# Kernel optimization log

Measured on AMD Instinct MI355X. Metric: run time of the kernel, lower is better.

## Reference

```python
import jax, jax.numpy as jnp
import numpy as np

N, NB, D, F, E, NUM_RBF = 50000, 256, 128, 16, 800000, 15
EPS = 1e-7
NEG = 0.01
MAX_LEN = 5.0


def _glorot(k, shape):
    return jax.random.normal(k, shape, dtype=jnp.float32) / np.float32(np.sqrt(shape[0]))


def setup_inputs() -> dict:
    key = jax.random.key(0)
    ks = jax.random.split(key, 32)
    inp = {}
    inp['h_A'] = jax.random.normal(ks[0], (N, D), jnp.float32)
    inp['v_A'] = jax.random.normal(ks[1], (N, F, 3), jnp.float32)
    inp['x_A'] = jax.random.normal(ks[2], (N, 3), jnp.float32) * 3.0
    inp['h_B'] = jax.random.normal(ks[3], (NB, D), jnp.float32)
    inp['mask'] = jnp.ones((N, NB), jnp.float32)
    inp['src'] = jax.random.randint(ks[4], (E,), 0, N, dtype=jnp.int32)
    inp['dst'] = jax.random.randint(ks[5], (E,), 0, N, dtype=jnp.int32)
    inp['rbf_k'] = jnp.array([0.5], jnp.float32)
    inp['W_rbf1'] = _glorot(ks[6], (NUM_RBF, D)); inp['b_rbf1'] = jnp.zeros((D,), jnp.float32)
    inp['W_rbf2'] = _glorot(ks[7], (NUM_RBF, F)); inp['b_rbf2'] = jnp.zeros((F,), jnp.float32)
    inp['W_rbf3'] = _glorot(ks[8], (NUM_RBF, F)); inp['b_rbf3'] = jnp.zeros((F,), jnp.float32)
    inp['vn1_W'] = _glorot(ks[9], (F, F)); inp['vn1_U'] = _glorot(ks[10], (F, F))
    inp['vn2_W'] = _glorot(ks[11], (F, F)); inp['vn2_U'] = _glorot(ks[12], (F, F))
    inp['vn3_W'] = _glorot(ks[13], (F, F)); inp['vn3_U'] = _glorot(ks[14], (F, F))
    inp['phi1_W'] = _glorot(ks[15], (D + F, D)); inp['phi1_b'] = jnp.zeros((D,), jnp.float32)
    inp['phi2_W'] = _glorot(ks[16], (D + F, F)); inp['phi2_b'] = jnp.zeros((F,), jnp.float32)
    inp['phi3_W'] = _glorot(ks[17], (D, F)); inp['phi3_b'] = jnp.zeros((F,), jnp.float32)
    inp['Wq'] = _glorot(ks[18], (D, D)); inp['Wk'] = _glorot(ks[19], (D, D))
    inp['Wv'] = _glorot(ks[20], (D, D)); inp['bv'] = jnp.zeros((D,), jnp.float32)
    inp['gru_Wih'] = _glorot(ks[21], (3 * D, 2 * D)) * 0.5
    inp['gru_Whh'] = _glorot(ks[22], (3 * D, D)) * 0.5
    inp['gru_bih'] = jnp.zeros((3 * D,), jnp.float32)
    inp['gru_bhh'] = jnp.zeros((3 * D,), jnp.float32)
    inp['vmlp_W1'] = _glorot(ks[23], (2 * F, 2 * F)); inp['vmlp_U1'] = _glorot(ks[24], (2 * F, 2 * F))
    inp['vmlp_W2'] = _glorot(ks[25], (F, 2 * F))
    return inp


def _forward(h_A, v_A, x_A, h_B, mask, src, dst, rbf_k, W_rbf1, b_rbf1, W_rbf2, b_rbf2,
             W_rbf3, b_rbf3, vn1_W, vn1_U, vn2_W, vn2_U, vn3_W, vn3_U, phi1_W, phi1_b,
             phi2_W, phi2_b, phi3_W, phi3_b, Wq, Wk, Wv, bv, gru_Wih, gru_Whh, gru_bih,
             gru_bhh, vmlp_W1, vmlp_U1, vmlp_W2):
    lrelu = lambda x: jax.nn.leaky_relu(x, NEG)

    def vn_relu(v, W, U):  # Vector Neuron linear + VN-ReLU; v: [n, f, 3]
        q = jnp.einsum('gf,nfc->ngc', W, v)
        k = jnp.einsum('gf,nfc->ngc', U, v)
        dot = jnp.sum(q * k, -1, keepdims=True)
        ksq = jnp.sum(k * k, -1, keepdims=True) + EPS
        return jnp.where(dot >= 0, q, q - (dot / ksq) * k)

    # --- per-node mixed scalar/vector features (generate_mixed_features) ---
    vnorm1 = jnp.linalg.norm(vn_relu(v_A, vn1_W, vn1_U), axis=2) + EPS  # [N,F]
    vnorm2 = jnp.linalg.norm(vn_relu(v_A, vn2_W, vn2_U), axis=2) + EPS
    hp = lrelu(jnp.concatenate([h_A, vnorm1], 1) @ phi1_W + phi1_b)     # [N,D]
    hpp = lrelu(jnp.concatenate([h_A, vnorm2], 1) @ phi2_W + phi2_b)    # [N,F]
    vp = vn_relu(v_A, vn3_W, vn3_U) * lrelu(h_A @ phi3_W + phi3_b)[:, :, None]  # [N,F,3]

    # --- cross attention A <- B ---
    q = lrelu(h_A @ Wq)
    kk = lrelu(h_B @ Wk)
    vv = h_B @ Wv + bv
    a = mask * (q @ kk.T) - 1000.0 * (1.0 - mask)                       # [N,NB]
    attn = jax.nn.softmax(a, axis=1) @ vv                               # [N,D]

    # --- edge-wise RBF expansion + point convolution messages ---
    r_ij = x_A[src] - x_A[dst]                                          # [E,3]
    rnorm = jnp.linalg.norm(r_ij, axis=1, keepdims=True)                # [E,1]
    centers = jnp.linspace(0.0, MAX_LEN, NUM_RBF, dtype=jnp.float32)
    rbf = jnp.exp(-jnp.square(rnorm - centers) * rbf_k)                 # [E,R]
    rbf_h = rbf @ W_rbf1 + b_rbf1                                       # [E,D]
    rbf_v1 = rbf @ W_rbf2 + b_rbf2                                      # [E,F]
    rbf_v2 = rbf @ W_rbf3 + b_rbf3                                      # [E,F]
    msg_h = rbf_h * hp[dst]                                             # [E,D]
    # einsum('ef,ef,ec->efc', rbf_v2, hpp_dst, r_ij)
    msg_v = rbf_v1[:, :, None] * vp[dst] + (rbf_v2 * hpp[dst])[:, :, None] * r_ij[:, None, :]

    # --- mean aggregation at destination nodes (update_all copy_e + mean) ---
    n_nodes = h_A.shape[0]
    cnt = jax.ops.segment_sum(jnp.ones((src.shape[0],), msg_h.dtype), dst, num_segments=n_nodes)
    den = jnp.maximum(cnt, 1.0)
    agg_h = jax.ops.segment_sum(msg_h, dst, num_segments=n_nodes) / den[:, None]
    agg_v = jax.ops.segment_sum(msg_v, dst, num_segments=n_nodes) / den[:, None, None]

    # --- GRUCell(2D, D): input = [h, cross_attn], hidden = aggregated message ---
    x_in = jnp.concatenate([h_A, attn], -1)                             # [N,2D]
    gi = x_in @ gru_Wih.T + gru_bih
    gh = agg_h @ gru_Whh.T + gru_bhh
    Dh = h_A.shape[1]
    r = jax.nn.sigmoid(gi[:, :Dh] + gh[:, :Dh])
    z = jax.nn.sigmoid(gi[:, Dh:2 * Dh] + gh[:, Dh:2 * Dh])
    n = jnp.tanh(gi[:, 2 * Dh:] + r * gh[:, 2 * Dh:])
    node_upd = h_A + ((1.0 - z) * n + z * agg_h)

    # --- vector update via Vector_MLP(2F -> F) with residual ---
    vin = jnp.concatenate([v_A, agg_v], axis=1)                         # [N,2F,3]
    vh = vn_relu(vin, vmlp_W1, vmlp_U1)
    v_evolved = v_A + jnp.einsum('gf,nfc->ngc', vmlp_W2, vh)            # [N,F,3]
    return v_evolved, node_upd


def reference(h_A, v_A, x_A, h_B, mask, src, dst, rbf_k, W_rbf1, b_rbf1, W_rbf2, b_rbf2,
              W_rbf3, b_rbf3, vn1_W, vn1_U, vn2_W, vn2_U, vn3_W, vn3_U, phi1_W, phi1_b,
              phi2_W, phi2_b, phi3_W, phi3_b, Wq, Wk, Wv, bv, gru_Wih, gru_Whh, gru_bih,
              gru_bhh, vmlp_W1, vmlp_U1, vmlp_W2):
    return _forward(h_A, v_A, x_A, h_B, mask, src, dst, rbf_k, W_rbf1, b_rbf1, W_rbf2,
                    b_rbf2, W_rbf3, b_rbf3, vn1_W, vn1_U, vn2_W, vn2_U, vn3_W, vn3_U,
                    phi1_W, phi1_b, phi2_W, phi2_b, phi3_W, phi3_b, Wq, Wk, Wv, bv,
                    gru_Wih, gru_Whh, gru_bih, gru_bhh, vmlp_W1, vmlp_U1, vmlp_W2)
```

## Files before the change

### kernel.cpp

```cpp
#include <hip/hip_runtime.h>
#include <math.h>

#define NN 50000
#define NBB 256
#define DD 128
#define FF 16
#define EE 800000
#define RR 15
#define EPSV 1e-7f
#define CSPACE (5.0f/14.0f)
#define NBLK 782

__device__ __forceinline__ float lrelu(float x){ return x >= 0.f ? x : 0.01f*x; }
__device__ __forceinline__ float sigmoidf_(float x){ return 1.f/(1.f+expf(-x)); }

typedef __bf16 bf16x8 __attribute__((ext_vector_type(8)));
typedef float f32x4 __attribute__((ext_vector_type(4)));

__device__ __forceinline__ unsigned short f2bf(float x){
    union { float f; unsigned int u; } a; a.f = x;
    unsigned int r = (a.u + 0x7fffu + ((a.u >> 16) & 1u)) >> 16;
    return (unsigned short)r;
}
__device__ __forceinline__ unsigned int pack2(float a, float b){
    return (unsigned int)f2bf(a) | ((unsigned int)f2bf(b) << 16);
}
// ... 261 lines not shown
                float* vo = vpO + (size_t)n*48 + lr*3;
                vo[0] = o[0]*gate; vo[1] = o[1]*gate; vo[2] = o[2]*gate;
            }
        }
    } else {
        float b2 = phi2b[lr];
        #pragma unroll
        for (int r4 = 0; r4 < 4; ++r4){
            int nl = (wv-4)*16 + lg*4 + r4;
            int n = n0 + nl;
            if (n < NN) hppO[(size_t)n*FF + lr] = lrelu(a23[r4] + b2);
        }
    }
}

__global__ __launch_bounds__(512, 4) void k_attn_mfma(
    const unsigned short* __restrict__ hAB, const unsigned short* __restrict__ pWq,
    const unsigned short* __restrict__ pKK, const unsigned short* __restrict__ pVV,
    const float* __restrict__ mask, unsigned short* __restrict__ attnB)
{
    __shared__ unsigned short sU[64*256];
    __shared__ float sMx[64][2];
    __shared__ float sSm[64][2];
    unsigned short* sX = sU;
    unsigned short* sQ = sU + 64*128;
    unsigned short* sP = sU;
    unsigned short* sImg = sU;
    int tid = threadIdx.x;
    int n0 = blockIdx.x*64;

    #pragma unroll
    for (int it = 0; it < 2; ++it){
        int i = tid + it*512;
        ((uint4*)sX)[i] = ((const uint4*)hAB)[(size_t)blockIdx.x*1024 + i];
    }
    __syncthreads();

    int wv = tid>>6, l = tid&63, lr = l&15, lg = l>>4;
    int rw = wv>>1, chh = wv&1;
    int rowA = rw*16 + lr;

    {
        f32x4 q[4];
        #pragma unroll
        for (int c = 0; c < 4; ++c) q[c] = (f32x4){0.f,0.f,0.f,0.f};
        for (int kt = 0; kt < 4; ++kt){
            bf16x8 a = ld8(&sX[rowA*128 + (((kt*4+lg) ^ (rowA&7))*8)]);
            #pragma unroll
            for (int c = 0; c < 4; ++c){
                bf16x8 b = ld8(pWq + (size_t)(((chh*4+c)*4 + kt)*512) + l*8);
                q[c] = __builtin_amdgcn_mfma_f32_16x16x32_bf16(a, b, q[c], 0, 0, 0);
            }
        }
        __syncthreads();
        #pragma unroll
        for (int c = 0; c < 4; ++c)
        #pragma unroll
        for (int r4 = 0; r4 < 4; ++r4){
            int row = rw*16 + lg*4 + r4;
            int col = chh*64 + c*16 + lr;
            int cb = col>>3;
            sQ[row*128 + ((cb ^ (row&7))*8) + (col&7)] = f2bf(lrelu(q[c][r4]));
        }
    }
    __syncthreads();

    f32x4 S[8];
    #pragma unroll
    for (int cl = 0; cl < 8; ++cl) S[cl] = (f32x4){0.f,0.f,0.f,0.f};
    for (int kt = 0; kt < 4; ++kt){
        bf16x8 a = ld8(&sQ[rowA*128 + (((kt*4+lg) ^ (rowA&7))*8)]);
        #pragma unroll
        for (int cl = 0; cl < 8; ++cl){
            bf16x8 b = ld8(pKK + (size_t)(((chh*8+cl)*4 + kt)*512) + l*8);
            S[cl] = __builtin_amdgcn_mfma_f32_16x16x32_bf16(a, b, S[cl], 0, 0, 0);
        }
    }
    float den[4];
    #pragma unroll
    for (int r4 = 0; r4 < 4; ++r4){
        int row = rw*16 + lg*4 + r4;
        int gn = n0 + row; if (gn > NN-1) gn = NN-1;
        float mx = -1e30f;
        #pragma unroll
        for (int cl = 0; cl < 8; ++cl){
            int col = chh*128 + cl*16 + lr;
            float m = mask[(size_t)gn*NBB + col];
            float s = m*S[cl][r4] - 1000.f*(1.f-m);
            S[cl][r4] = s;
            mx = fmaxf(mx, s);
        }
        mx = fmaxf(mx, __shfl_xor(mx, 1));
        mx = fmaxf(mx, __shfl_xor(mx, 2));
        mx = fmaxf(mx, __shfl_xor(mx, 4));
        mx = fmaxf(mx, __shfl_xor(mx, 8));
        if (lr == 0) sMx[row][chh] = mx;
    }
    __syncthreads();
    #pragma unroll
    for (int r4 = 0; r4 < 4; ++r4){
        int row = rw*16 + lg*4 + r4;
        float m = fmaxf(sMx[row][0], sMx[row][1]);
        float sm = 0.f;
        #pragma unroll
        for (int cl = 0; cl < 8; ++cl){
            float p = expf(S[cl][r4] - m);
            S[cl][r4] = p;
            sm += p;
        }
        sm += __shfl_xor(sm, 1);
        sm += __shfl_xor(sm, 2);
        sm += __shfl_xor(sm, 4);
        sm += __shfl_xor(sm, 8);
        if (lr == 0) sSm[row][chh] = sm;
    }
    __syncthreads();
    #pragma unroll
    for (int r4 = 0; r4 < 4; ++r4){
        int row = rw*16 + lg*4 + r4;
        den[r4] = sSm[row][0] + sSm[row][1];
    }
    #pragma unroll
    for (int cl = 0; cl < 8; ++cl)
    #pragma unroll
    for (int r4 = 0; r4 < 4; ++r4){
        int row = rw*16 + lg*4 + r4;
        int col = chh*128 + cl*16 + lr;
        int cb = col>>3;
        sP[row*256 + ((cb ^ (row&7))*8) + (col&7)] = f2bf(S[cl][r4]);
    }
    __syncthreads();

    f32x4 O[4];
    #pragma unroll
    for (int c = 0; c < 4; ++c) O[c] = (f32x4){0.f,0.f,0.f,0.f};
    for (int kt = 0; kt < 8; ++kt){
        bf16x8 a = ld8(&sP[rowA*256 + (((kt*4+lg) ^ (rowA&7))*8)]);
        #pragma unroll
        for (int c = 0; c < 4; ++c){
            bf16x8 b = ld8(pVV + (size_t)(((chh*4+c)*8 + kt)*512) + l*8);
            O[c] = __builtin_amdgcn_mfma_f32_16x16x32_bf16(a, b, O[c], 0, 0, 0);
        }
    }
    __syncthreads();
    #pragma unroll
    for (int c = 0; c < 4; ++c)
    #pragma unroll
    for (int r4 = 0; r4 < 4; ++r4){
        int row = rw*16 + lg*4 + r4;
        int col = chh*64 + c*16 + lr;
        sImg[row*128 + (((col>>3) ^ (row&7))*8) + (col&7)] = f2bf(O[c][r4] / den[r4]);
    }
    __syncthreads();
    #pragma unroll
    for (int it = 0; it < 2; ++it){
        int i = tid + it*512;
        ((uint4*)attnB)[(size_t)blockIdx.x*1024 + i] = ((const uint4*)sImg)[i];
    }
}

__global__ __launch_bounds__(256) void k_hist(const int* __restrict__ dst, int* __restrict__ deg){
    int e = blockIdx.x*256 + threadIdx.x;
    if (e < EE) atomicAdd(&deg[dst[e]], 1);
}

__global__ __launch_bounds__(256) void k_scan1(const int* __restrict__ deg,
                                               int* __restrict__ excl, int* __restrict__ bsum){
    __shared__ int s[256];
    int tid = threadIdx.x;
    int i = blockIdx.x*256 + tid;
    int v = (i < NN) ? deg[i] : 0;
    s[tid] = v;
    __syncthreads();
    for (int o = 1; o < 256; o <<= 1){
        int t = 0;
// ... 28 lines not shown
        start[i] = st;
        cursor[i] = st;
    }
    if (i == 0) start[NN] = EE;
}

__global__ __launch_bounds__(256) void k_scatter(const int* __restrict__ src,
                                                 const int* __restrict__ dst,
                                                 int* __restrict__ cursor, int* __restrict__ esrc){
    int e = blockIdx.x*256 + threadIdx.x;
    if (e >= EE) return;
    int pos = atomicAdd(&cursor[dst[e]], 1);
    esrc[pos] = src[e];
}

__global__ __launch_bounds__(256) void k_gather(const int* __restrict__ start,
                                                const int* __restrict__ esrc,
                                                const float* __restrict__ xA,
                                                const float* __restrict__ rbf_k,
                                                float* __restrict__ acc)
{
    int gt = blockIdx.x*256 + threadIdx.x;
    int n = gt >> 2, sub = gt & 3;
    if (n >= NN) return;
    float kc = rbf_k[0];
    float xd0 = xA[n*3+0], xd1 = xA[n*3+1], xd2 = xA[n*3+2];
    float a[64];
    #pragma unroll
    for (int i = 0; i < 64; ++i) a[i] = 0.f;
    int b0 = start[n], b1 = start[n+1];
    for (int i = b0 + sub; i < b1; i += 4){
        int s = esrc[i];
        float r0 = xA[s*3+0]-xd0, r1 = xA[s*3+1]-xd1, r2 = xA[s*3+2]-xd2;
        float rn = sqrtf(r0*r0+r1*r1+r2*r2);
        a[0] += 1.f;
        a[16] += r0; a[17] += r1; a[18] += r2;
        #pragma unroll
        for (int q = 0; q < RR; ++q){
            float df = rn - (float)q*CSPACE;
            float rb = expf(-df*df*kc);
            a[1+q] += rb;
            a[19+q*3+0] += rb*r0;
            a[19+q*3+1] += rb*r1;
            a[19+q*3+2] += rb*r2;
        }
    }
    #pragma unroll
    for (int i = 0; i < 64; ++i){
        a[i] += __shfl_xor(a[i], 1);
        a[i] += __shfl_xor(a[i], 2);
    }
    float4* o = (float4*)(acc + (size_t)n*64);
    #pragma unroll
    for (int i = 0; i < 4; ++i){
        int idx = sub*4 + i;
        o[idx] = make_float4(a[4*idx], a[4*idx+1], a[4*idx+2], a[4*idx+3]);
    }
}

__global__ __launch_bounds__(512) void k_gru_mfma(
    const unsigned short* __restrict__ hAB, const unsigned short* __restrict__ attnB,
    const unsigned short* __restrict__ hpB, const float* __restrict__ acc,
    const unsigned short* __restrict__ pWr1,
    const unsigned short* __restrict__ pWih, const unsigned short* __restrict__ pWhh,
    const float* __restrict__ bih, const float* __restrict__ bhh,
    float* __restrict__ outNode)
{
    __shared__ unsigned short sX[64*256];
    __shared__ unsigned short sGm[64*128];
    __shared__ float sCnt[64];
    unsigned short* sM = sGm;
    int tid = threadIdx.x;
    int n0 = blockIdx.x*64;

    #pragma unroll
    for (int it = 0; it < 2; ++it){
        int i = tid + it*512;
        uint4 v = ((const uint4*)hAB)[(size_t)blockIdx.x*1024 + i];
        int row = i >> 4, p = i & 15;
        *(uint4*)&sX[row*256 + p*8] = v;
    }
    #pragma unroll
    for (int it = 0; it < 2; ++it){
        int i = tid + it*512;
        uint4 v = ((const uint4*)attnB)[(size_t)blockIdx.x*1024 + i];
        int row = i >> 4, p = i & 15;
        *(uint4*)&sX[row*256 + 128 + p*8] = v;
    }
    #pragma unroll
    for (int it = 0; it < 4; ++it){
        int i = tid + it*512;
        int row = i >> 5, k = i & 31;
        int gn = n0 + row; if (gn > NN-1) gn = NN-1;
        float v = (k < 16) ? acc[(size_t)gn*64 + k] : 0.f;
        sM[row*40 + k] = f2bf(v);
        if (k == 0) sCnt[row] = v;
    }
    __syncthreads();

    int wv = tid >> 6, l = tid & 63;
    int lr = l & 15, lg = l >> 4;
    int col = wv*16 + lr;

    {
        f32x4 sv[4];
        #pragma unroll
        for (int rt = 0; rt < 4; ++rt) sv[rt] = (f32x4){0.f,0.f,0.f,0.f};
        bf16x8 b = ld8(pWr1 + (size_t)wv*512 + l*8);
        #pragma unroll
        for (int rt = 0; rt < 4; ++rt){
            int row = rt*16 + lr;
            bf16x8 a = ld8(&sM[row*40 + lg*8]);
            sv[rt] = __builtin_amdgcn_mfma_f32_16x16x32_bf16(a, b, sv[rt], 0, 0, 0);
        }
        __syncthreads();
        #pragma unroll
        for (int rt = 0; rt < 4; ++rt){
            #pragma unroll
            for (int r4 = 0; r4 < 4; ++r4){
                int row = rt*16 + lg*4 + r4;
                int gn = n0 + row; if (gn > NN-1) gn = NN-1;
                float cnt = sCnt[row];
                float den = fmaxf(cnt, 1.f);
                float g = bf2f(hpB[(size_t)gn*DD + col]) * sv[rt][r4] / den;
                sGm[row*128 + (((col>>3) ^ (row&7))*8) + (col&7)] = f2bf(g);
            }
        }
    }
    __syncthreads();

    f32x4 aR[4], aZ[4], aNI[4], aNH[4];
    #pragma unroll
    for (int rt = 0; rt < 4; ++rt){
        aR[rt] = (f32x4){0.f,0.f,0.f,0.f};
        aZ[rt] = (f32x4){0.f,0.f,0.f,0.f};
        aNI[rt] = (f32x4){0.f,0.f,0.f,0.f};
        aNH[rt] = (f32x4){0.f,0.f,0.f,0.f};
    }
    const unsigned short* bR = pWih + ((size_t)(0*8 + wv)*8)*512 + l*8;
    const unsigned short* bZ = pWih + ((size_t)(1*8 + wv)*8)*512 + l*8;
    const unsigned short* bN = pWih + ((size_t)(2*8 + wv)*8)*512 + l*8;
    for (int kt = 0; kt < 8; ++kt){
        bf16x8 br_ = ld8(bR + kt*512);
        bf16x8 bz_ = ld8(bZ + kt*512);
        bf16x8 bn_ = ld8(bN + kt*512);
        #pragma unroll
        for (int rt = 0; rt < 4; ++rt){
            int rowA = rt*16 + lr;
            bf16x8 a = ld8(&sX[rowA*256 + (((kt*4 + lg) ^ (rowA&7))*8)]);
            aR[rt]  = __builtin_amdgcn_mfma_f32_16x16x32_bf16(a, br_, aR[rt], 0, 0, 0);
            aZ[rt]  = __builtin_amdgcn_mfma_f32_16x16x32_bf16(a, bz_, aZ[rt], 0, 0, 0);
            aNI[rt] = __builtin_amdgcn_mfma_f32_16x16x32_bf16(a, bn_, aNI[rt], 0, 0, 0);
        }
    }
    const unsigned short* cR = pWhh + ((size_t)(0*8 + wv)*4)*512 + l*8;
    const unsigned short* cZ = pWhh + ((size_t)(1*8 + wv)*4)*512 + l*8;
    const unsigned short* cN = pWhh + ((size_t)(2*8 + wv)*4)*512 + l*8;
    for (int kt = 0; kt < 4; ++kt){
        bf16x8 br_ = ld8(cR + kt*512);
        bf16x8 bz_ = ld8(cZ + kt*512);
        bf16x8 bn_ = ld8(cN + kt*512);
        #pragma unroll
        for (int rt = 0; rt < 4; ++rt){
            int rowA = rt*16 + lr;
            bf16x8 a = ld8(&sGm[rowA*128 + (((kt*4 + lg) ^ (rowA&7))*8)]);
            aR[rt]  = __builtin_amdgcn_mfma_f32_16x16x32_bf16(a, br_, aR[rt], 0, 0, 0);
            aZ[rt]  = __builtin_amdgcn_mfma_f32_16x16x32_bf16(a, bz_, aZ[rt], 0, 0, 0);
            aNH[rt] = __builtin_amdgcn_mfma_f32_16x16x32_bf16(a, bn_, aNH[rt], 0, 0, 0);
        }
    }

    float b_r = bih[col] + bhh[col];
    float b_z = bih[DD+col] + bhh[DD+col];
    float b_ni = bih[2*DD+col];
    float b_nh = bhh[2*DD+col];
    #pragma unroll
    for (int rt = 0; rt < 4; ++rt){
        #pragma unroll
        for (int r4 = 0; r4 < 4; ++r4){
            int nl = rt*16 + lg*4 + r4;
            int n = n0 + nl;
            if (n < NN){
                float rg = sigmoidf_(aR[rt][r4] + b_r);
                float zg = sigmoidf_(aZ[rt][r4] + b_z);
                float ng = tanhf(aNI[rt][r4] + b_ni + rg*(aNH[rt][r4] + b_nh));
                float sg = bf2f(sGm[nl*128 + (((col>>3) ^ (nl&7))*8) + (col&7)]);
                float h = bf2f(sX[nl*256 + (((col>>3) ^ (nl&7))*8) + (col&7)]);
                outNode[(size_t)n*DD + col] = h + (1.f-zg)*ng + zg*sg;
            }
        }
    }
}

__global__ __launch_bounds__(256) void k_vec(
    const float* __restrict__ vA, const float* __restrict__ vp,
    const float* __restrict__ hpp, const float* __restrict__ acc,
    const float* __restrict__ Wr2, const float* __restrict__ br2,
    const float* __restrict__ Wr3, const float* __restrict__ br3,
    const float* __restrict__ W1, const float* __restrict__ U1,
    const float* __restrict__ W2, float* __restrict__ outV)
{
    __shared__ float sW1[32*32], sU1[32*32], sW2[16*32];
    __shared__ float sWr2[RR*FF], sWr3[RR*FF];
    __shared__ float sVin[8][32][3];
    __shared__ float sVh[8][32][3];
    __shared__ float sAcc[8][64];
    __shared__ float sVA[8][48];
    int tid = threadIdx.x;
    for (int i = tid; i < 1024; i += 256){ sW1[i]=W1[i]; sU1[i]=U1[i]; }
    for (int i = tid; i < 512; i += 256) sW2[i]=W2[i];
    for (int i = tid; i < RR*FF; i += 256){ sWr2[i]=Wr2[i]; sWr3[i]=Wr3[i]; }
    int n0 = blockIdx.x*8;
    for (int i = tid; i < 8*64; i += 256) sAcc[i/64][i%64] = acc[(size_t)n0*64 + i];
    for (int i = tid; i < 8*48; i += 256) sVA[i/48][i%48] = vA[(size_t)n0*48 + i];
    __syncthreads();
    int t = tid >> 5, g = tid & 31;
    int n = n0 + t;
    if (g < 16){
        int f = g;
        float cnt = sAcc[t][0];
        float den = fmaxf(cnt, 1.f);
        float s1 = cnt*br2[f];
        #pragma unroll
        for (int r = 0; r < RR; ++r) s1 += sAcc[t][1+r]*sWr2[r*FF+f];
        float hpv = hpp[(size_t)n*FF+f];
        float b3 = br3[f];
        #pragma unroll
        for (int c = 0; c < 3; ++c){
            float s2 = b3*sAcc[t][16+c];
            #pragma unroll
            for (int r = 0; r < RR; ++r) s2 += sAcc[t][19+r*3+c]*sWr3[r*FF+f];
            float aggv = (vp[(size_t)n*48 + f*3 + c]*s1 + hpv*s2)/den;
            sVin[t][FF+f][c] = aggv;
            sVin[t][f][c] = sVA[t][f*3+c];
        }
    }
    __syncthreads();
    {
        float q0=0,q1=0,q2=0,k0=0,k1=0,k2=0;
        #pragma unroll
        for (int ff = 0; ff < 32; ++ff){
            int f = (ff + g) & 31;
            float w = sW1[g*32+f], u = sU1[g*32+f];
            float v0=sVin[t][f][0], v1=sVin[t][f][1], v2=sVin[t][f][2];
            q0+=w*v0;q1+=w*v1;q2+=w*v2;
            k0+=u*v0;k1+=u*v1;k2+=u*v2;
        }
        float dot=q0*k0+q1*k1+q2*k2;
        float ksq=k0*k0+k1*k1+k2*k2+EPSV;
        float s = dot>=0.f?0.f:dot/ksq;
        sVh[t][g][0]=q0-s*k0; sVh[t][g][1]=q1-s*k1; sVh[t][g][2]=q2-s*k2;
    }
    __syncthreads();
    if (g < 16){
        float o0=sVA[t][g*3+0], o1=sVA[t][g*3+1], o2=sVA[t][g*3+2];
        #pragma unroll
        for (int ff = 0; ff < 32; ++ff){
            int f = (ff + g) & 31;
            float w = sW2[g*32+f];
            o0 += w*sVh[t][f][0];
            o1 += w*sVh[t][f][1];
            o2 += w*sVh[t][f][2];
        }
        outV[(size_t)n*48 + g*3 + 0] = o0;
        outV[(size_t)n*48 + g*3 + 1] = o1;
        outV[(size_t)n*48 + g*3 + 2] = o2;
    }
}

extern "C" void kernel_launch(void* const* d_in, const int* in_sizes, int n_in,
                              void* d_out, int out_size, void* d_ws, size_t ws_size,
                              hipStream_t stream)
{
    const float* hA   = (const float*)d_in[0];
    const float* vA   = (const float*)d_in[1];
    const float* xA   = (const float*)d_in[2];
    const float* hB   = (const float*)d_in[3];
// ... 55 lines not shown
    int* esrc   = (int*)ws;  ws += EE;

    float* outV = (float*)d_out;
    float* outH = (float*)d_out + (size_t)NN*FF*3;

    const int NB_SCAN = (NN + 255)/256;

    k_prep<<<512, 256, 0, stream>>>(Wih, Whh, Wq, phi1W, phi2W, phi3W, Wr1, br1,
                                    hB, Wk, Wv, bv,
                                    pWih, pWhh, pWq, pPhi1, pPhi2, pPhi3, pWr1,
                                    pKK, pVV, deg);
    k_hist<<<(EE+255)/256, 256, 0, stream>>>(dst, deg);
    k_scan1<<<NB_SCAN, 256, 0, stream>>>(deg, excl, bsum);
    k_scan23<<<NB_SCAN, 256, 0, stream>>>(excl, bsum, NB_SCAN, startN, cursor);
    k_scatter<<<(EE+255)/256, 256, 0, stream>>>(src, dst, cursor, esrc);
    k_gather<<<(NN*4+255)/256, 256, 0, stream>>>(startN, esrc, xA, rbfk, acc);
    k_node<<<NBLK, 512, 0, stream>>>(hA, vA, vn1W, vn1U, vn2W, vn2U, vn3W, vn3U,
                                     pPhi1, phi1b, pPhi2, phi2b, pPhi3, phi3b,
                                     hpB, hpp, vp, hAB);
    k_attn_mfma<<<NBLK, 512, 0, stream>>>(hAB, pWq, pKK, pVV, mask, attnB);
    k_gru_mfma<<<NBLK, 512, 0, stream>>>(hAB, attnB, hpB, acc, pWr1,
                                         pWih, pWhh, bih, bhh, outH);
    k_vec<<<NN/8, 256, 0, stream>>>(vA, vp, hpp, acc, Wr2, br2, Wr3, br3, W1, U1, W2, outV);
}
```

Before: 336.8 us.

## Merge independent kernels into shared launches via block-range dispatch

Combines the edge gather with the attention kernel, and the GRU with the vector-update kernel, into single launches. Block index ranges pick which workload each block runs. The goal is to cut launch count and let independent work fill the GPU at the same time, removing tail idle time between kernels. In exchange, each fused kernel uses the larger of the two register and shared-memory footprints, and the attention part loses its launch_bounds occupancy hint, which may lower occupancy.

Result: slower. 344.0 us (+2.1%).

```diff
diff --git a/kernel.cpp b/kernel.cpp
--- a/kernel.cpp
+++ b/kernel.cpp
@@ -10,6 +10,8 @@
 #define EPSV 1e-7f
 #define CSPACE (5.0f/14.0f)
 #define NBLK 782
+#define NGA 391
+#define NVB 3125
 
 __device__ __forceinline__ float lrelu(float x){ return x >= 0.f ? x : 0.01f*x; }
 __device__ __forceinline__ float sigmoidf_(float x){ return 1.f/(1.f+expf(-x)); }
@@ -301,151 +303,6 @@
     }
 }
 
-__global__ __launch_bounds__(512, 4) void k_attn_mfma(
-    const unsigned short* __restrict__ hAB, const unsigned short* __restrict__ pWq,
-    const unsigned short* __restrict__ pKK, const unsigned short* __restrict__ pVV,
-    const float* __restrict__ mask, unsigned short* __restrict__ attnB)
-{
-    __shared__ unsigned short sU[64*256];
-    __shared__ float sMx[64][2];
-    __shared__ float sSm[64][2];
-    unsigned short* sX = sU;
-    unsigned short* sQ = sU + 64*128;
-    unsigned short* sP = sU;
-    unsigned short* sImg = sU;
-    int tid = threadIdx.x;
-    int n0 = blockIdx.x*64;
-
-    #pragma unroll
-    for (int it = 0; it < 2; ++it){
-        int i = tid + it*512;
-        ((uint4*)sX)[i] = ((const uint4*)hAB)[(size_t)blockIdx.x*1024 + i];
-    }
-    __syncthreads();
-
-    int wv = tid>>6, l = tid&63, lr = l&15, lg = l>>4;
-    int rw = wv>>1, chh = wv&1;
-    int rowA = rw*16 + lr;
-
-    {
-        f32x4 q[4];
-        #pragma unroll
-        for (int c = 0; c < 4; ++c) q[c] = (f32x4){0.f,0.f,0.f,0.f};
-        for (int kt = 0; kt < 4; ++kt){
-            bf16x8 a = ld8(&sX[rowA*128 + (((kt*4+lg) ^ (rowA&7))*8)]);
-            #pragma unroll
-            for (int c = 0; c < 4; ++c){
-                bf16x8 b = ld8(pWq + (size_t)(((chh*4+c)*4 + kt)*512) + l*8);
-                q[c] = __builtin_amdgcn_mfma_f32_16x16x32_bf16(a, b, q[c], 0, 0, 0);
-            }
-        }
-        __syncthreads();
-        #pragma unroll
-        for (int c = 0; c < 4; ++c)
-        #pragma unroll
-        for (int r4 = 0; r4 < 4; ++r4){
-            int row = rw*16 + lg*4 + r4;
-            int col = chh*64 + c*16 + lr;
-            int cb = col>>3;
-            sQ[row*128 + ((cb ^ (row&7))*8) + (col&7)] = f2bf(lrelu(q[c][r4]));
-        }
-    }
-    __syncthreads();
-
-    f32x4 S[8];
-    #pragma unroll
-    for (int cl = 0; cl < 8; ++cl) S[cl] = (f32x4){0.f,0.f,0.f,0.f};
-    for (int kt = 0; kt < 4; ++kt){
-        bf16x8 a = ld8(&sQ[rowA*128 + (((kt*4+lg) ^ (rowA&7))*8)]);
-        #pragma unroll
-        for (int cl = 0; cl < 8; ++cl){
-            bf16x8 b = ld8(pKK + (size_t)(((chh*8+cl)*4 + kt)*512) + l*8);
-            S[cl] = __builtin_amdgcn_mfma_f32_16x16x32_bf16(a, b, S[cl], 0, 0, 0);
-        }
-    }
-    float den[4];
-    #pragma unroll
-    for (int r4 = 0; r4 < 4; ++r4){
-        int row = rw*16 + lg*4 + r4;
-        int gn = n0 + row; if (gn > NN-1) gn = NN-1;
-        float mx = -1e30f;
-        #pragma unroll
-        for (int cl = 0; cl < 8; ++cl){
-            int col = chh*128 + cl*16 + lr;
-            float m = mask[(size_t)gn*NBB + col];
-            float s = m*S[cl][r4] - 1000.f*(1.f-m);
-            S[cl][r4] = s;
-            mx = fmaxf(mx, s);
-        }
-        mx = fmaxf(mx, __shfl_xor(mx, 1));
-        mx = fmaxf(mx, __shfl_xor(mx, 2));
-        mx = fmaxf(mx, __shfl_xor(mx, 4));
-        mx = fmaxf(mx, __shfl_xor(mx, 8));
-        if (lr == 0) sMx[row][chh] = mx;
-    }
-    __syncthreads();
-    #pragma unroll
-    for (int r4 = 0; r4 < 4; ++r4){
-        int row = rw*16 + lg*4 + r4;
-        float m = fmaxf(sMx[row][0], sMx[row][1]);
-        float sm = 0.f;
-        #pragma unroll
-        for (int cl = 0; cl < 8; ++cl){
-            float p = expf(S[cl][r4] - m);
-            S[cl][r4] = p;
-            sm += p;
-        }
-        sm += __shfl_xor(sm, 1);
-        sm += __shfl_xor(sm, 2);
-        sm += __shfl_xor(sm, 4);
-        sm += __shfl_xor(sm, 8);
-        if (lr == 0) sSm[row][chh] = sm;
-    }
-    __syncthreads();
-    #pragma unroll
-    for (int r4 = 0; r4 < 4; ++r4){
-        int row = rw*16 + lg*4 + r4;
-        den[r4] = sSm[row][0] + sSm[row][1];
-    }
-    #pragma unroll
-    for (int cl = 0; cl < 8; ++cl)
-    #pragma unroll
-    for (int r4 = 0; r4 < 4; ++r4){
-        int row = rw*16 + lg*4 + r4;
-        int col = chh*128 + cl*16 + lr;
-        int cb = col>>3;
-        sP[row*256 + ((cb ^ (row&7))*8) + (col&7)] = f2bf(S[cl][r4]);
-    }
-    __syncthreads();
-
-    f32x4 O[4];
-    #pragma unroll
-    for (int c = 0; c < 4; ++c) O[c] = (f32x4){0.f,0.f,0.f,0.f};
-    for (int kt = 0; kt < 8; ++kt){
-        bf16x8 a = ld8(&sP[rowA*256 + (((kt*4+lg) ^ (rowA&7))*8)]);
-        #pragma unroll
-        for (int c = 0; c < 4; ++c){
-            bf16x8 b = ld8(pVV + (size_t)(((chh*4+c)*8 + kt)*512) + l*8);
-            O[c] = __builtin_amdgcn_mfma_f32_16x16x32_bf16(a, b, O[c], 0, 0, 0);
-        }
-    }
-    __syncthreads();
-    #pragma unroll
-    for (int c = 0; c < 4; ++c)
-    #pragma unroll
-    for (int r4 = 0; r4 < 4; ++r4){
-        int row = rw*16 + lg*4 + r4;
-        int col = chh*64 + c*16 + lr;
-        sImg[row*128 + (((col>>3) ^ (row&7))*8) + (col&7)] = f2bf(O[c][r4] / den[r4]);
-    }
-    __syncthreads();
-    #pragma unroll
-    for (int it = 0; it < 2; ++it){
-        int i = tid + it*512;
-        ((uint4*)attnB)[(size_t)blockIdx.x*1024 + i] = ((const uint4*)sImg)[i];
-    }
-}
-
 __global__ __launch_bounds__(256) void k_hist(const int* __restrict__ dst, int* __restrict__ deg){
     int e = blockIdx.x*256 + threadIdx.x;
     if (e < EE) atomicAdd(&deg[dst[e]], 1);
@@ -504,225 +361,374 @@
     esrc[pos] = src[e];
 }
 
-__global__ __launch_bounds__(256) void k_gather(const int* __restrict__ start,
-                                                const int* __restrict__ esrc,
-                                                const float* __restrict__ xA,
-                                                const float* __restrict__ rbf_k,
-                                                float* __restrict__ acc)
+__global__ __launch_bounds__(512) void k_ga_attn(
+    const int* __restrict__ start, const int* __restrict__ esrc,
+    const float* __restrict__ xA, const float* __restrict__ rbf_k,
+    float* __restrict__ acc,
+    const unsigned short* __restrict__ hAB, const unsigned short* __restrict__ pWq,
+    const unsigned short* __restrict__ pKK, const unsigned short* __restrict__ pVV,
+    const float* __restrict__ mask, unsigned short* __restrict__ attnB)
 {
-    int gt = blockIdx.x*256 + threadIdx.x;
-    int n = gt >> 2, sub = gt & 3;
-    if (n >= NN) return;
-    float kc = rbf_k[0];
-    float xd0 = xA[n*3+0], xd1 = xA[n*3+1], xd2 = xA[n*3+2];
-    float a[64];
-    #pragma unroll
-    for (int i = 0; i < 64; ++i) a[i] = 0.f;
-    int b0 = start[n], b1 = start[n+1];
-    for (int i = b0 + sub; i < b1; i += 4){
-        int s = esrc[i];
-        float r0 = xA[s*3+0]-xd0, r1 = xA[s*3+1]-xd1, r2 = xA[s*3+2]-xd2;
-        float rn = sqrtf(r0*r0+r1*r1+r2*r2);
-        a[0] += 1.f;
-        a[16] += r0; a[17] += r1; a[18] += r2;
-        #pragma unroll
-        for (int q = 0; q < RR; ++q){
-            float df = rn - (float)q*CSPACE;
-            float rb = expf(-df*df*kc);
-            a[1+q] += rb;
-            a[19+q*3+0] += rb*r0;
-            a[19+q*3+1] += rb*r1;
-            a[19+q*3+2] += rb*r2;
-        }
-    }
-    #pragma unroll
-    for (int i = 0; i < 64; ++i){
-        a[i] += __shfl_xor(a[i], 1);
-        a[i] += __shfl_xor(a[i], 2);
-    }
-    float4* o = (float4*)(acc + (size_t)n*64);
-    #pragma unroll
-    for (int i = 0; i < 4; ++i){
-        int idx = sub*4 + i;
-        o[idx] = make_float4(a[4*idx], a[4*idx+1], a[4*idx+2], a[4*idx+3]);
-    }
-}
-
-__global__ __launch_bounds__(512) void k_gru_mfma(
+    __shared__ __align__(16) unsigned char smem[33792];
+    int tid = threadIdx.x;
+    if (blockIdx.x < NGA){
+        int gt = blockIdx.x*512 + tid;
+        int n = gt >> 2, sub = gt & 3;
+        if (n >= NN) return;
+        float kc = rbf_k[0];
+        float xd0 = xA[n*3+0], xd1 = xA[n*3+1], xd2 = xA[n*3+2];
+        float a[64];
+        #pragma unroll
+        for (int i = 0; i < 64; ++i) a[i] = 0.f;
+        int b0 = start[n], b1 = start[n+1];
+        for (int i = b0 + sub; i < b1; i += 4){
+            int s = esrc[i];
+            float r0 = xA[s*3+0]-xd0, r1 = xA[s*3+1]-xd1, r2 = xA[s*3+2]-xd2;
+            float rn = sqrtf(r0*r0+r1*r1+r2*r2);
+            a[0] += 1.f;
+            a[16] += r0; a[17] += r1; a[18] += r2;
+            #pragma unroll
+            for (int q = 0; q < RR; ++q){
+                float df = rn - (float)q*CSPACE;
+                float rb = expf(-df*df*kc);
+                a[1+q] += rb;
+                a[19+q*3+0] += rb*r0;
+                a[19+q*3+1] += rb*r1;
+                a[19+q*3+2] += rb*r2;
+            }
+        }
+        #pragma unroll
+        for (int i = 0; i < 64; ++i){
+            a[i] += __shfl_xor(a[i], 1);
+            a[i] += __shfl_xor(a[i], 2);
+        }
+        float4* o = (float4*)(acc + (size_t)n*64);
+        #pragma unroll
+        for (int i = 0; i < 4; ++i){
+            int idx = sub*4 + i;
+            o[idx] = make_float4(a[4*idx], a[4*idx+1], a[4*idx+2], a[4*idx+3]);
+        }
+        return;
+    }
+    int ab = blockIdx.x - NGA;
+    unsigned short* sU = (unsigned short*)smem;
+    float* sMx = (float*)(smem + 32768);
+    float* sSm = (float*)(smem + 33280);
+    unsigned short* sX = sU;
+    unsigned short* sQ = sU + 64*128;
+    unsigned short* sP = sU;
+    unsigned short* sImg = sU;
+    int n0 = ab*64;
+
+    #pragma unroll
+    for (int it = 0; it < 2; ++it){
+        int i = tid + it*512;
+        ((uint4*)sX)[i] = ((const uint4*)hAB)[(size_t)ab*1024 + i];
+    }
+    __syncthreads();
+
+    int wv = tid>>6, l = tid&63, lr = l&15, lg = l>>4;
+    int rw = wv>>1, chh = wv&1;
+    int rowA = rw*16 + lr;
+
+    {
+        f32x4 q[4];
+        #pragma unroll
+        for (int c = 0; c < 4; ++c) q[c] = (f32x4){0.f,0.f,0.f,0.f};
+        for (int kt = 0; kt < 4; ++kt){
+            bf16x8 a = ld8(&sX[rowA*128 + (((kt*4+lg) ^ (rowA&7))*8)]);
+            #pragma unroll
+            for (int c = 0; c < 4; ++c){
+                bf16x8 b = ld8(pWq + (size_t)(((chh*4+c)*4 + kt)*512) + l*8);
+                q[c] = __builtin_amdgcn_mfma_f32_16x16x32_bf16(a, b, q[c], 0, 0, 0);
+            }
+        }
+        __syncthreads();
+        #pragma unroll
+        for (int c = 0; c < 4; ++c)
+        #pragma unroll
+        for (int r4 = 0; r4 < 4; ++r4){
+            int row = rw*16 + lg*4 + r4;
+            int col = chh*64 + c*16 + lr;
+            int cb = col>>3;
+            sQ[row*128 + ((cb ^ (row&7))*8) + (col&7)] = f2bf(lrelu(q[c][r4]));
+        }
+    }
+    __syncthreads();
+
+    f32x4 S[8];
+    #pragma unroll
+    for (int cl = 0; cl < 8; ++cl) S[cl] = (f32x4){0.f,0.f,0.f,0.f};
+    for (int kt = 0; kt < 4; ++kt){
+        bf16x8 a = ld8(&sQ[rowA*128 + (((kt*4+lg) ^ (rowA&7))*8)]);
+        #pragma unroll
+        for (int cl = 0; cl < 8; ++cl){
+            bf16x8 b = ld8(pKK + (size_t)(((chh*8+cl)*4 + kt)*512) + l*8);
+            S[cl] = __builtin_amdgcn_mfma_f32_16x16x32_bf16(a, b, S[cl], 0, 0, 0);
+        }
+    }
+    float den[4];
+    #pragma unroll
+    for (int r4 = 0; r4 < 4; ++r4){
+        int row = rw*16 + lg*4 + r4;
+        int gn = n0 + row; if (gn > NN-1) gn = NN-1;
+        float mx = -1e30f;
+        #pragma unroll
+        for (int cl = 0; cl < 8; ++cl){
+            int col = chh*128 + cl*16 + lr;
+            float m = mask[(size_t)gn*NBB + col];
+            float s = m*S[cl][r4] - 1000.f*(1.f-m);
+            S[cl][r4] = s;
+            mx = fmaxf(mx, s);
+        }
+        mx = fmaxf(mx, __shfl_xor(mx, 1));
+        mx = fmaxf(mx, __shfl_xor(mx, 2));
+        mx = fmaxf(mx, __shfl_xor(mx, 4));
+        mx = fmaxf(mx, __shfl_xor(mx, 8));
+        if (lr == 0) sMx[row*2+chh] = mx;
+    }
+    __syncthreads();
+    #pragma unroll
+    for (int r4 = 0; r4 < 4; ++r4){
+        int row = rw*16 + lg*4 + r4;
+        float m = fmaxf(sMx[row*2+0], sMx[row*2+1]);
+        float sm = 0.f;
+        #pragma unroll
+        for (int cl = 0; cl < 8; ++cl){
+            float p = expf(S[cl][r4] - m);
+            S[cl][r4] = p;
+            sm += p;
+        }
+        sm += __shfl_xor(sm, 1);
+        sm += __shfl_xor(sm, 2);
+        sm += __shfl_xor(sm, 4);
+        sm += __shfl_xor(sm, 8);
+        if (lr == 0) sSm[row*2+chh] = sm;
+    }
+    __syncthreads();
+    #pragma unroll
+    for (int r4 = 0; r4 < 4; ++r4){
+        int row = rw*16 + lg*4 + r4;
+        den[r4] = sSm[row*2+0] + sSm[row*2+1];
+    }
+    #pragma unroll
+    for (int cl = 0; cl < 8; ++cl)
+    #pragma unroll
+    for (int r4 = 0; r4 < 4; ++r4){
+        int row = rw*16 + lg*4 + r4;
+        int col = chh*128 + cl*16 + lr;
+        int cb = col>>3;
+        sP[row*256 + ((cb ^ (row&7))*8) + (col&7)] = f2bf(S[cl][r4]);
+    }
+    __syncthreads();
+
+    f32x4 O[4];
+    #pragma unroll
+    for (int c = 0; c < 4; ++c) O[c] = (f32x4){0.f,0.f,0.f,0.f};
+    for (int kt = 0; kt < 8; ++kt){
+        bf16x8 a = ld8(&sP[rowA*256 + (((kt*4+lg) ^ (rowA&7))*8)]);
+        #pragma unroll
+        for (int c = 0; c < 4; ++c){
+            bf16x8 b = ld8(pVV + (size_t)(((chh*4+c)*8 + kt)*512) + l*8);
+            O[c] = __builtin_amdgcn_mfma_f32_16x16x32_bf16(a, b, O[c], 0, 0, 0);
+        }
+    }
+    __syncthreads();
+    #pragma unroll
+    for (int c = 0; c < 4; ++c)
+    #pragma unroll
+    for (int r4 = 0; r4 < 4; ++r4){
+        int row = rw*16 + lg*4 + r4;
+        int col = chh*64 + c*16 + lr;
+        sImg[row*128 + (((col>>3) ^ (row&7))*8) + (col&7)] = f2bf(O[c][r4] / den[r4]);
+    }
+    __syncthreads();
+    #pragma unroll
+    for (int it = 0; it < 2; ++it){
+        int i = tid + it*512;
+        ((uint4*)attnB)[(size_t)ab*1024 + i] = ((const uint4*)sImg)[i];
+    }
+}
+
+__global__ __launch_bounds__(512) void k_gru_vec(
     const unsigned short* __restrict__ hAB, const unsigned short* __restrict__ attnB,
     const unsigned short* __restrict__ hpB, const float* __restrict__ acc,
     const unsigned short* __restrict__ pWr1,
     const unsigned short* __restrict__ pWih, const unsigned short* __restrict__ pWhh,
     const float* __restrict__ bih, const float* __restrict__ bhh,
-    float* __restrict__ outNode)
-{
-    __shared__ unsigned short sX[64*256];
-    __shared__ unsigned short sGm[64*128];
-    __shared__ float sCnt[64];
-    unsigned short* sM = sGm;
-    int tid = threadIdx.x;
-    int n0 = blockIdx.x*64;
-
-    #pragma unroll
-    for (int it = 0; it < 2; ++it){
-        int i = tid + it*512;
-        uint4 v = ((const uint4*)hAB)[(size_t)blockIdx.x*1024 + i];
-        int row = i >> 4, p = i & 15;
-        *(uint4*)&sX[row*256 + p*8] = v;
-    }
-    #pragma unroll
-    for (int it = 0; it < 2; ++it){
-        int i = tid + it*512;
-        uint4 v = ((const uint4*)attnB)[(size_t)blockIdx.x*1024 + i];
-        int row = i >> 4, p = i & 15;
-        *(uint4*)&sX[row*256 + 128 + p*8] = v;
-    }
-    #pragma unroll
-    for (int it = 0; it < 4; ++it){
-        int i = tid + it*512;
-        int row = i >> 5, k = i & 31;
-        int gn = n0 + row; if (gn > NN-1) gn = NN-1;
-        float v = (k < 16) ? acc[(size_t)gn*64 + k] : 0.f;
-        sM[row*40 + k] = f2bf(v);
-        if (k == 0) sCnt[row] = v;
-    }
-    __syncthreads();
-
-    int wv = tid >> 6, l = tid & 63;
-    int lr = l & 15, lg = l >> 4;
-    int col = wv*16 + lr;
-
-    {
-        f32x4 sv[4];
-        #pragma unroll
-        for (int rt = 0; rt < 4; ++rt) sv[rt] = (f32x4){0.f,0.f,0.f,0.f};
-        bf16x8 b = ld8(pWr1 + (size_t)wv*512 + l*8);
-        #pragma unroll
-        for (int rt = 0; rt < 4; ++rt){
-            int row = rt*16 + lr;
-            bf16x8 a = ld8(&sM[row*40 + lg*8]);
-            sv[rt] = __builtin_amdgcn_mfma_f32_16x16x32_bf16(a, b, sv[rt], 0, 0, 0);
-        }
-        __syncthreads();
-        #pragma unroll
-        for (int rt = 0; rt < 4; ++rt){
-            #pragma unroll
-            for (int r4 = 0; r4 < 4; ++r4){
-                int row = rt*16 + lg*4 + r4;
-                int gn = n0 + row; if (gn > NN-1) gn = NN-1;
-                float cnt = sCnt[row];
-                float den = fmaxf(cnt, 1.f);
-                float g = bf2f(hpB[(size_t)gn*DD + col]) * sv[rt][r4] / den;
-                sGm[row*128 + (((col>>3) ^ (row&7))*8) + (col&7)] = f2bf(g);
-            }
-        }
-    }
-    __syncthreads();
-
-    f32x4 aR[4], aZ[4], aNI[4], aNH[4];
-    #pragma unroll
-    for (int rt = 0; rt < 4; ++rt){
-        aR[rt] = (f32x4){0.f,0.f,0.f,0.f};
-        aZ[rt] = (f32x4){0.f,0.f,0.f,0.f};
-        aNI[rt] = (f32x4){0.f,0.f,0.f,0.f};
-        aNH[rt] = (f32x4){0.f,0.f,0.f,0.f};
-    }
-    const unsigned short* bR = pWih + ((size_t)(0*8 + wv)*8)*512 + l*8;
-    const unsigned short* bZ = pWih + ((size_t)(1*8 + wv)*8)*512 + l*8;
-    const unsigned short* bN = pWih + ((size_t)(2*8 + wv)*8)*512 + l*8;
-    for (int kt = 0; kt < 8; ++kt){
-        bf16x8 br_ = ld8(bR + kt*512);
-        bf16x8 bz_ = ld8(bZ + kt*512);
-        bf16x8 bn_ = ld8(bN + kt*512);
-        #pragma unroll
-        for (int rt = 0; rt < 4; ++rt){
-            int rowA = rt*16 + lr;
-            bf16x8 a = ld8(&sX[rowA*256 + (((kt*4 + lg) ^ (rowA&7))*8)]);
-            aR[rt]  = __builtin_amdgcn_mfma_f32_16x16x32_bf16(a, br_, aR[rt], 0, 0, 0);
-            aZ[rt]  = __builtin_amdgcn_mfma_f32_16x16x32_bf16(a, bz_, aZ[rt], 0, 0, 0);
-            aNI[rt] = __builtin_amdgcn_mfma_f32_16x16x32_bf16(a, bn_, aNI[rt], 0, 0, 0);
-        }
-    }
-    const unsigned short* cR = pWhh + ((size_t)(0*8 + wv)*4)*512 + l*8;
-    const unsigned short* cZ = pWhh + ((size_t)(1*8 + wv)*4)*512 + l*8;
-    const unsigned short* cN = pWhh + ((size_t)(2*8 + wv)*4)*512 + l*8;
-    for (int kt = 0; kt < 4; ++kt){
-        bf16x8 br_ = ld8(cR + kt*512);
-        bf16x8 bz_ = ld8(cZ + kt*512);
-        bf16x8 bn_ = ld8(cN + kt*512);
-        #pragma unroll
-        for (int rt = 0; rt < 4; ++rt){
-            int rowA = rt*16 + lr;
-            bf16x8 a = ld8(&sGm[rowA*128 + (((kt*4 + lg) ^ (rowA&7))*8)]);
-            aR[rt]  = __builtin_amdgcn_mfma_f32_16x16x32_bf16(a, br_, aR[rt], 0, 0, 0);
-            aZ[rt]  = __builtin_amdgcn_mfma_f32_16x16x32_bf16(a, bz_, aZ[rt], 0, 0, 0);
-            aNH[rt] = __builtin_amdgcn_mfma_f32_16x16x32_bf16(a, bn_, aNH[rt], 0, 0, 0);
-        }
-    }
-
-    float b_r = bih[col] + bhh[col];
-    float b_z = bih[DD+col] + bhh[DD+col];
-    float b_ni = bih[2*DD+col];
-    float b_nh = bhh[2*DD+col];
-    #pragma unroll
-    for (int rt = 0; rt < 4; ++rt){
-        #pragma unroll
-        for (int r4 = 0; r4 < 4; ++r4){
-            int nl = rt*16 + lg*4 + r4;
-            int n = n0 + nl;
-            if (n < NN){
-                float rg = sigmoidf_(aR[rt][r4] + b_r);
-                float zg = sigmoidf_(aZ[rt][r4] + b_z);
-                float ng = tanhf(aNI[rt][r4] + b_ni + rg*(aNH[rt][r4] + b_nh));
-                float sg = bf2f(sGm[nl*128 + (((col>>3) ^ (nl&7))*8) + (col&7)]);
-                float h = bf2f(sX[nl*256 + (((col>>3) ^ (nl&7))*8) + (col&7)]);
-                outNode[(size_t)n*DD + col] = h + (1.f-zg)*ng + zg*sg;
-            }
-        }
-    }
-}
-
-__global__ __launch_bounds__(256) void k_vec(
+    float* __restrict__ outNode,
     const float* __restrict__ vA, const float* __restrict__ vp,
-    const float* __restrict__ hpp, const float* __restrict__ acc,
+    const float* __restrict__ hpp,
     const float* __restrict__ Wr2, const float* __restrict__ br2,
     const float* __restrict__ Wr3, const float* __restrict__ br3,
     const float* __restrict__ W1, const float* __restrict__ U1,
     const float* __restrict__ W2, float* __restrict__ outV)
 {
-    __shared__ float sW1[32*32], sU1[32*32], sW2[16*32];
-    __shared__ float sWr2[RR*FF], sWr3[RR*FF];
-    __shared__ float sVin[8][32][3];
-    __shared__ float sVh[8][32][3];
-    __shared__ float sAcc[8][64];
-    __shared__ float sVA[8][48];
+    __shared__ __align__(16) unsigned char smem[49408];
     int tid = threadIdx.x;
-    for (int i = tid; i < 1024; i += 256){ sW1[i]=W1[i]; sU1[i]=U1[i]; }
-    for (int i = tid; i < 512; i += 256) sW2[i]=W2[i];
-    for (int i = tid; i < RR*FF; i += 256){ sWr2[i]=Wr2[i]; sWr3[i]=Wr3[i]; }
-    int n0 = blockIdx.x*8;
-    for (int i = tid; i < 8*64; i += 256) sAcc[i/64][i%64] = acc[(size_t)n0*64 + i];
-    for (int i = tid; i < 8*48; i += 256) sVA[i/48][i%48] = vA[(size_t)n0*48 + i];
+    if (blockIdx.x < NBLK){
+        unsigned short* sX  = (unsigned short*)smem;
+        unsigned short* sGm = (unsigned short*)(smem + 32768);
+        float* sCnt = (float*)(smem + 49152);
+        unsigned short* sM = sGm;
+        int n0 = blockIdx.x*64;
+
+        #pragma unroll
+        for (int it = 0; it < 2; ++it){
+            int i = tid + it*512;
+            uint4 v = ((const uint4*)hAB)[(size_t)blockIdx.x*1024 + i];
+            int row = i >> 4, p = i & 15;
+            *(uint4*)&sX[row*256 + p*8] = v;
+        }
+        #pragma unroll
+        for (int it = 0; it < 2; ++it){
+            int i = tid + it*512;
+            uint4 v = ((const uint4*)attnB)[(size_t)blockIdx.x*1024 + i];
+            int row = i >> 4, p = i & 15;
+            *(uint4*)&sX[row*256 + 128 + p*8] = v;
+        }
+        #pragma unroll
+        for (int it = 0; it < 4; ++it){
+            int i = tid + it*512;
+            int row = i >> 5, k = i & 31;
+            int gn = n0 + row; if (gn > NN-1) gn = NN-1;
+            float v = (k < 16) ? acc[(size_t)gn*64 + k] : 0.f;
+            sM[row*40 + k] = f2bf(v);
+            if (k == 0) sCnt[row] = v;
+        }
+        __syncthreads();
+
+        int wv = tid >> 6, l = tid & 63;
+        int lr = l & 15, lg = l >> 4;
+        int col = wv*16 + lr;
+
+        {
+            f32x4 sv[4];
+            #pragma unroll
+            for (int rt = 0; rt < 4; ++rt) sv[rt] = (f32x4){0.f,0.f,0.f,0.f};
+            bf16x8 b = ld8(pWr1 + (size_t)wv*512 + l*8);
+            #pragma unroll
+            for (int rt = 0; rt < 4; ++rt){
+                int row = rt*16 + lr;
+                bf16x8 a = ld8(&sM[row*40 + lg*8]);
+                sv[rt] = __builtin_amdgcn_mfma_f32_16x16x32_bf16(a, b, sv[rt], 0, 0, 0);
+            }
+            __syncthreads();
+            #pragma unroll
+            for (int rt = 0; rt < 4; ++rt){
+                #pragma unroll
+                for (int r4 = 0; r4 < 4; ++r4){
+                    int row = rt*16 + lg*4 + r4;
+                    int gn = n0 + row; if (gn > NN-1) gn = NN-1;
+                    float cnt = sCnt[row];
+                    float den = fmaxf(cnt, 1.f);
+                    float g = bf2f(hpB[(size_t)gn*DD + col]) * sv[rt][r4] / den;
+                    sGm[row*128 + (((col>>3) ^ (row&7))*8) + (col&7)] = f2bf(g);
+                }
+            }
+        }
+        __syncthreads();
+
+        f32x4 aR[4], aZ[4], aNI[4], aNH[4];
+        #pragma unroll
+        for (int rt = 0; rt < 4; ++rt){
+            aR[rt] = (f32x4){0.f,0.f,0.f,0.f};
+            aZ[rt] = (f32x4){0.f,0.f,0.f,0.f};
+            aNI[rt] = (f32x4){0.f,0.f,0.f,0.f};
+            aNH[rt] = (f32x4){0.f,0.f,0.f,0.f};
+        }
+        const unsigned short* bR = pWih + ((size_t)(0*8 + wv)*8)*512 + l*8;
+        const unsigned short* bZ = pWih + ((size_t)(1*8 + wv)*8)*512 + l*8;
+        const unsigned short* bN = pWih + ((size_t)(2*8 + wv)*8)*512 + l*8;
+        for (int kt = 0; kt < 8; ++kt){
+            bf16x8 br_ = ld8(bR + kt*512);
+            bf16x8 bz_ = ld8(bZ + kt*512);
+            bf16x8 bn_ = ld8(bN + kt*512);
+            #pragma unroll
+            for (int rt = 0; rt < 4; ++rt){
+                int rowA = rt*16 + lr;
+                bf16x8 a = ld8(&sX[rowA*256 + (((kt*4 + lg) ^ (rowA&7))*8)]);
+                aR[rt]  = __builtin_amdgcn_mfma_f32_16x16x32_bf16(a, br_, aR[rt], 0, 0, 0);
+                aZ[rt]  = __builtin_amdgcn_mfma_f32_16x16x32_bf16(a, bz_, aZ[rt], 0, 0, 0);
+                aNI[rt] = __builtin_amdgcn_mfma_f32_16x16x32_bf16(a, bn_, aNI[rt], 0, 0, 0);
+            }
+        }
+        const unsigned short* cR = pWhh + ((size_t)(0*8 + wv)*4)*512 + l*8;
+        const unsigned short* cZ = pWhh + ((size_t)(1*8 + wv)*4)*512 + l*8;
+        const unsigned short* cN = pWhh + ((size_t)(2*8 + wv)*4)*512 + l*8;
+        for (int kt = 0; kt < 4; ++kt){
+            bf16x8 br_ = ld8(cR + kt*512);
+            bf16x8 bz_ = ld8(cZ + kt*512);
+            bf16x8 bn_ = ld8(cN + kt*512);
+            #pragma unroll
+            for (int rt = 0; rt < 4; ++rt){
+                int rowA = rt*16 + lr;
+                bf16x8 a = ld8(&sGm[rowA*128 + (((kt*4 + lg) ^ (rowA&7))*8)]);
+                aR[rt]  = __builtin_amdgcn_mfma_f32_16x16x32_bf16(a, br_, aR[rt], 0, 0, 0);
+                aZ[rt]  = __builtin_amdgcn_mfma_f32_16x16x32_bf16(a, bz_, aZ[rt], 0, 0, 0);
+                aNH[rt] = __builtin_amdgcn_mfma_f32_16x16x32_bf16(a, bn_, aNH[rt], 0, 0, 0);
+            }
+        }
+
+        float b_r = bih[col] + bhh[col];
+        float b_z = bih[DD+col] + bhh[DD+col];
+        float b_ni = bih[2*DD+col];
+        float b_nh = bhh[2*DD+col];
+        #pragma unroll
+        for (int rt = 0; rt < 4; ++rt){
+            #pragma unroll
+            for (int r4 = 0; r4 < 4; ++r4){
+                int nl = rt*16 + lg*4 + r4;
+                int n = n0 + nl;
+                if (n < NN){
+                    float rg = sigmoidf_(aR[rt][r4] + b_r);
+                    float zg = sigmoidf_(aZ[rt][r4] + b_z);
+                    float ng = tanhf(aNI[rt][r4] + b_ni + rg*(aNH[rt][r4] + b_nh));
+                    float sg = bf2f(sGm[nl*128 + (((col>>3) ^ (nl&7))*8) + (col&7)]);
+                    float h = bf2f(sX[nl*256 + (((col>>3) ^ (nl&7))*8) + (col&7)]);
+                    outNode[(size_t)n*DD + col] = h + (1.f-zg)*ng + zg*sg;
+                }
+            }
+        }
+        return;
+    }
+    int vb = blockIdx.x - NBLK;
+    float* fb = (float*)smem;
+    float* sW1 = fb;
+    float* sU1 = fb + 1024;
+    float* sW2 = fb + 2048;
+    float* sWr2 = fb + 2560;
+    float* sWr3 = fb + 2800;
+    float* sVin = fb + 3040;
+    float* sVh  = fb + 4576;
+    float* sAcc = fb + 6112;
+    float* sVA  = fb + 7136;
+    int n0 = vb*16;
+    for (int i = tid; i < 1024; i += 512){ sW1[i]=W1[i]; sU1[i]=U1[i]; }
+    for (int i = tid; i < 512; i += 512) sW2[i]=W2[i];
+    for (int i = tid; i < 240; i += 512){ sWr2[i]=Wr2[i]; sWr3[i]=Wr3[i]; }
+    for (int i = tid; i < 1024; i += 512) sAcc[i] = acc[(size_t)n0*64 + i];
+    for (int i = tid; i < 768; i += 512) sVA[i] = vA[(size_t)n0*48 + i];
     __syncthreads();
     int t = tid >> 5, g = tid & 31;
     int n = n0 + t;
     if (g < 16){
         int f = g;
-        float cnt = sAcc[t][0];
+        float cnt = sAcc[t*64];
         float den = fmaxf(cnt, 1.f);
         float s1 = cnt*br2[f];
         #pragma unroll
-        for (int r = 0; r < RR; ++r) s1 += sAcc[t][1+r]*sWr2[r*FF+f];
+        for (int r = 0; r < RR; ++r) s1 += sAcc[t*64+1+r]*sWr2[r*FF+f];
         float hpv = hpp[(size_t)n*FF+f];
         float b3 = br3[f];
         #pragma unroll
         for (int c = 0; c < 3; ++c){
-            float s2 = b3*sAcc[t][16+c];
-            #pragma unroll
-            for (int r = 0; r < RR; ++r) s2 += sAcc[t][19+r*3+c]*sWr3[r*FF+f];
+            float s2 = b3*sAcc[t*64+16+c];
+            #pragma unroll
+            for (int r = 0; r < RR; ++r) s2 += sAcc[t*64+19+r*3+c]*sWr3[r*FF+f];
             float aggv = (vp[(size_t)n*48 + f*3 + c]*s1 + hpv*s2)/den;
-            sVin[t][FF+f][c] = aggv;
-            sVin[t][f][c] = sVA[t][f*3+c];
+            sVin[(t*32+FF+f)*3+c] = aggv;
+            sVin[(t*32+f)*3+c] = sVA[t*48 + f*3 + c];
         }
     }
     __syncthreads();
@@ -732,25 +738,25 @@
         for (int ff = 0; ff < 32; ++ff){
             int f = (ff + g) & 31;
             float w = sW1[g*32+f], u = sU1[g*32+f];
-            float v0=sVin[t][f][0], v1=sVin[t][f][1], v2=sVin[t][f][2];
+            float v0=sVin[(t*32+f)*3+0], v1=sVin[(t*32+f)*3+1], v2=sVin[(t*32+f)*3+2];
             q0+=w*v0;q1+=w*v1;q2+=w*v2;
             k0+=u*v0;k1+=u*v1;k2+=u*v2;
         }
         float dot=q0*k0+q1*k1+q2*k2;
         float ksq=k0*k0+k1*k1+k2*k2+EPSV;
         float s = dot>=0.f?0.f:dot/ksq;
-        sVh[t][g][0]=q0-s*k0; sVh[t][g][1]=q1-s*k1; sVh[t][g][2]=q2-s*k2;
+        sVh[(t*32+g)*3+0]=q0-s*k0; sVh[(t*32+g)*3+1]=q1-s*k1; sVh[(t*32+g)*3+2]=q2-s*k2;
     }
     __syncthreads();
     if (g < 16){
-        float o0=sVA[t][g*3+0], o1=sVA[t][g*3+1], o2=sVA[t][g*3+2];
+        float o0=sVA[t*48+g*3+0], o1=sVA[t*48+g*3+1], o2=sVA[t*48+g*3+2];
         #pragma unroll
         for (int ff = 0; ff < 32; ++ff){
             int f = (ff + g) & 31;
             float w = sW2[g*32+f];
-            o0 += w*sVh[t][f][0];
-            o1 += w*sVh[t][f][1];
-            o2 += w*sVh[t][f][2];
+            o0 += w*sVh[(t*32+f)*3+0];
+            o1 += w*sVh[(t*32+f)*3+1];
+            o2 += w*sVh[(t*32+f)*3+2];
         }
         outV[(size_t)n*48 + g*3 + 0] = o0;
         outV[(size_t)n*48 + g*3 + 1] = o1;
@@ -836,12 +842,13 @@
     k_scan1<<<NB_SCAN, 256, 0, stream>>>(deg, excl, bsum);
     k_scan23<<<NB_SCAN, 256, 0, stream>>>(excl, bsum, NB_SCAN, startN, cursor);
     k_scatter<<<(EE+255)/256, 256, 0, stream>>>(src, dst, cursor, esrc);
-    k_gather<<<(NN*4+255)/256, 256, 0, stream>>>(startN, esrc, xA, rbfk, acc);
     k_node<<<NBLK, 512, 0, stream>>>(hA, vA, vn1W, vn1U, vn2W, vn2U, vn3W, vn3U,
                                      pPhi1, phi1b, pPhi2, phi2b, pPhi3, phi3b,
                                      hpB, hpp, vp, hAB);
-    k_attn_mfma<<<NBLK, 512, 0, stream>>>(hAB, pWq, pKK, pVV, mask, attnB);
-    k_gru_mfma<<<NBLK, 512, 0, stream>>>(hAB, attnB, hpB, acc, pWr1,
-                                         pWih, pWhh, bih, bhh, outH);
-    k_vec<<<NN/8, 256, 0, stream>>>(vA, vp, hpp, acc, Wr2, br2, Wr3, br3, W1, U1, W2, outV);
-}
+    k_ga_attn<<<NGA + NBLK, 512, 0, stream>>>(startN, esrc, xA, rbfk, acc,
+                                              hAB, pWq, pKK, pVV, mask, attnB);
+    k_gru_vec<<<NBLK + NVB, 512, 0, stream>>>(hAB, attnB, hpB, acc, pWr1,
+                                              pWih, pWhh, bih, bhh, outH,
+                                              vA, vp, hpp, Wr2, br2, Wr3, br3,
+                                              W1, U1, W2, outV);
+}
```
